# Kernel tuning notes

Measured on AMD Instinct MI355X. Metric: run time of the kernel, lower is better.

## Reference

```python
import jax, jax.numpy as jnp
import numpy as np

# B batch, SEQ encoder len, LDEC = label_len + pred_len = SEQ//2 + PRED decoder len
B, SEQ, PRED, LABEL = 4, 4096, 2048, 2048
NF, D, H, E, M, MA = 21, 512, 8, 64, 64, 25  # feats, d_model, heads, head_dim, modes, moving_avg
DFF, NLAYERS = 2048, 2
LDEC = LABEL + PRED

def pos_emb(L, d):
    pos = jnp.arange(L, dtype=jnp.float32)[:, None]
    div = jnp.exp(jnp.arange(0, d, 2, dtype=jnp.float32) * (-np.log(10000.0) / d))
    pe = jnp.zeros((L, d), jnp.float32)
    pe = pe.at[:, 0::2].set(jnp.sin(pos * div))
    pe = pe.at[:, 1::2].set(jnp.cos(pos * div))
    return pe

def circular_conv3(x, W):
    # torch Conv1d(k=3, padding=1, padding_mode='circular', bias=False); x:(B,L,Cin) W:(Cout,Cin,3)
    L = x.shape[1]
    xp = jnp.concatenate([x[:, -1:], x, x[:, :1]], axis=1)
    return xp[:, :L] @ W[:, :, 0].T + xp[:, 1:L + 1] @ W[:, :, 1].T + xp[:, 2:] @ W[:, :, 2].T

def series_decomp(x):
    # moving_avg: replicate-pad ends by (MA-1)//2, then AvgPool1d(MA, stride=1)
    p = (MA - 1) // 2
    xp = jnp.concatenate([jnp.repeat(x[:, :1], p, 1), x, jnp.repeat(x[:, -1:], p, 1)], axis=1)
    ma = jax.lax.reduce_window(xp, 0.0, jax.lax.add, (1, MA, 1), (1, 1, 1), 'VALID') / MA
    return x - ma, ma

def layer_norm(x, g, b, eps=1e-5):
    mu = x.mean(-1, keepdims=True)
    var = ((x - mu) ** 2).mean(-1, keepdims=True)
    return (x - mu) / jnp.sqrt(var + eps) * g + b

def my_layernorm(x, g, b):
    # my_Layernorm: LayerNorm minus its mean over the time axis
    xh = layer_norm(x, g, b)
    return xh - xh.mean(1, keepdims=True)

def to_c(Wf):
    return jax.lax.complex(Wf[..., 0], Wf[..., 1])

def fourier_block(q, Wf):
    # q:(B,L,H,E) -> out:(B,H,E,L); 'low' mode selection keeps the first M rfft bins
    x = jnp.transpose(q, (0, 2, 3, 1))
    L = x.shape[-1]
    xf = jnp.fft.rfft(x, axis=-1)[..., :M]
    of = jnp.einsum('bhim,hiom->bhom', xf, to_c(Wf))
    of = jnp.pad(of, ((0, 0), (0, 0), (0, 0), (0, L // 2 + 1 - M)))
    return jnp.fft.irfft(of, n=L, axis=-1)

def fourier_cross(q, k, Wf):
    # FourierCrossAttention with activation='tanh'; v is unused (as in torch)
    xq = jnp.transpose(q, (0, 2, 3, 1))
    xk = jnp.transpose(k, (0, 2, 3, 1))
    Lq = xq.shape[-1]
    qf = jnp.fft.rfft(xq, axis=-1)[..., :M]
    kf = jnp.fft.rfft(xk, axis=-1)[..., :M]
    s = jnp.tanh(jnp.einsum('bhex,bhey->bhxy', qf, kf))  # complex tanh
    o = jnp.einsum('bhxy,bhey->bhex', s, kf)
    ow = jnp.einsum('bhex,heox->bhox', o, to_c(Wf))
    of = jnp.pad(ow, ((0, 0), (0, 0), (0, 0), (0, Lq // 2 + 1 - M)))
    return jnp.fft.irfft(of / (D * D), n=Lq, axis=-1)  # / in_channels / out_channels

def attn_layer(xq, xkv, W4, b4, inner):
    Bq, Lq, Lk = xq.shape[0], xq.shape[1], xkv.shape[1]
    q = (xq @ W4[0].T + b4[0]).reshape(Bq, Lq, H, E)
    k = (xkv @ W4[1].T + b4[1]).reshape(Bq, Lk, H, E)
    v = (xkv @ W4[2].T + b4[2]).reshape(Bq, Lk, H, E)  # projected but unused by Fourier attention
    out = inner(q, k, v).reshape(Bq, Lq, H * E)  # replicates torch .view(B, L, -1) on contiguous (B,H,E,L)
    return out @ W4[3].T + b4[3]

def encoder_layer(x, W4, b4, Wf, W1, W2):
    x, _ = series_decomp(x + attn_layer(x, x, W4, b4, lambda q, k, v: fourier_block(q, Wf)))
    y = jax.nn.gelu(x @ W1.T, approximate=False) @ W2.T  # 1x1 convs == linear, no bias
    res, _ = series_decomp(x + y)
    return res

def decoder_layer(x, cross, Ws4, bs4, Wc4, bc4, Wf_self, Wf_cross, W1, W2, Wproj):
    x, t1 = series_decomp(x + attn_layer(x, x, Ws4, bs4, lambda q, k, v: fourier_block(q, Wf_self)))
    x, t2 = series_decomp(x + attn_layer(x, cross, Wc4, bc4, lambda q, k, v: fourier_cross(q, k, Wf_cross)))
    y = jax.nn.gelu(x @ W1.T, approximate=False) @ W2.T
    x, t3 = series_decomp(x + y)
    return x, circular_conv3(t1 + t2 + t3, Wproj)

def forward(x_enc, enc_emb_W, dec_emb_W, enc_qkvo_W, enc_qkvo_b, enc_ffn_W1, enc_ffn_W2, enc_fourier_W, enc_norm_g, enc_norm_b, dec_qkvo_W, dec_qkvo_b, dec_ffn_W1, dec_ffn_W2, dec_self_fourier_W, dec_cross_fourier_W, dec_trend_proj_W, dec_norm_g, dec_norm_b, final_W, final_b):
    mean = jnp.repeat(x_enc.mean(1, keepdims=True), PRED, axis=1)
    seasonal_init, trend_init = series_decomp(x_enc)
    trend_init = jnp.concatenate([trend_init[:, -LABEL:], mean], axis=1)  # (B,LDEC,NF)
    seasonal_init = jnp.pad(seasonal_init[:, -LABEL:], ((0, 0), (0, PRED), (0, 0)))
    enc_out = circular_conv3(x_enc, enc_emb_W) + pos_emb(SEQ, D)   # x_mark is None -> value + pos emb
    dec_out = circular_conv3(seasonal_init, dec_emb_W) + pos_emb(LDEC, D)
    for l in range(NLAYERS):  # encoder Fourier weights are a single shared module in torch
        enc_out = encoder_layer(enc_out, enc_qkvo_W[l], enc_qkvo_b[l], enc_fourier_W, enc_ffn_W1[l], enc_ffn_W2[l])
    enc_out = my_layernorm(enc_out, enc_norm_g, enc_norm_b)
    x, residual_trend = decoder_layer(dec_out, enc_out, dec_qkvo_W[0], dec_qkvo_b[0], dec_qkvo_W[1], dec_qkvo_b[1], dec_self_fourier_W, dec_cross_fourier_W, dec_ffn_W1, dec_ffn_W2, dec_trend_proj_W)
    trend = trend_init + residual_trend
    seasonal = my_layernorm(x, dec_norm_g, dec_norm_b) @ final_W.T + final_b
    return (trend + seasonal)[:, -PRED:, :]

def setup_inputs():
    ks = iter(jax.random.split(jax.random.key(0), 24))
    rn = lambda shape, s=0.02: jax.random.normal(next(ks), shape, jnp.float32) * s
    rf = lambda shape: jax.random.uniform(next(ks), shape, jnp.float32) / (D * D)  # torch.rand * 1/(in*out), complex split into (...,2)
    return {
        'x_enc': jax.random.normal(next(ks), (B, SEQ, NF), jnp.float32),
        'time': jnp.zeros((1,), jnp.int32),
        'dec_time': jnp.zeros((1,), jnp.int32),
        'enc_emb_W': rn((D, NF, 3)),
        'dec_emb_W': rn((D, NF, 3)),
        'enc_qkvo_W': rn((NLAYERS, 4, D, D)),
        'enc_qkvo_b': rn((NLAYERS, 4, D)),
        'enc_ffn_W1': rn((NLAYERS, DFF, D)),
        'enc_ffn_W2': rn((NLAYERS, D, DFF)),
        'enc_fourier_W': rf((H, E, E, M, 2)),
        'enc_norm_g': jnp.ones((D,), jnp.float32),
        'enc_norm_b': jnp.zeros((D,), jnp.float32),
        'dec_qkvo_W': rn((2, 4, D, D)),
        'dec_qkvo_b': rn((2, 4, D)),
        'dec_ffn_W1': rn((DFF, D)),
        'dec_ffn_W2': rn((D, DFF)),
        'dec_self_fourier_W': rf((H, E, E, M, 2)),
        'dec_cross_fourier_W': rf((H, E, E, M, 2)),
        'dec_trend_proj_W': rn((NF, D, 3)),
        'dec_norm_g': jnp.ones((D,), jnp.float32),
        'dec_norm_b': jnp.zeros((D,), jnp.float32),
        'final_W': rn((NF, D)),
        'final_b': jnp.zeros((NF,), jnp.float32),
    }

def reference(x_enc, time, dec_time, enc_emb_W, dec_emb_W, enc_qkvo_W, enc_qkvo_b, enc_ffn_W1, enc_ffn_W2, enc_fourier_W, enc_norm_g, enc_norm_b, dec_qkvo_W, dec_qkvo_b, dec_ffn_W1, dec_ffn_W2, dec_self_fourier_W, dec_cross_fourier_W, dec_trend_proj_W, dec_norm_g, dec_norm_b, final_W, final_b):
    # torch forward sets time = dec_time = None immediately; they are ignored
    return forward(x_enc, enc_emb_W, dec_emb_W, enc_qkvo_W, enc_qkvo_b, enc_ffn_W1, enc_ffn_W2, enc_fourier_W, enc_norm_g, enc_norm_b, dec_qkvo_W, dec_qkvo_b, dec_ffn_W1, dec_ffn_W2, dec_self_fourier_W, dec_cross_fourier_W, dec_trend_proj_W, dec_norm_g, dec_norm_b, final_W, final_b)
```

## Files before the change

kernel.cpp:

```cpp
#include <hip/hip_runtime.h>
#include <hip/hip_bf16.h>
#include <math.h>

namespace {

constexpr int NB    = 4;
constexpr int L     = 4096;
constexpr int PRED  = 2048;
constexpr int LABEL = 2048;
constexpr int NF    = 21;
constexpr int Dm    = 512;
constexpr int NH    = 8;
constexpr int NE    = 64;
constexpr int NM    = 64;
constexpr int DFF   = 2048;
constexpr float TWOPI = 6.283185307179586f;

typedef __attribute__((ext_vector_type(8))) short s16x8;
typedef __attribute__((ext_vector_type(4))) short s16x4;
typedef __attribute__((ext_vector_type(4))) float f32x4;

__device__ inline short f2b(float f) {
  __hip_bfloat16 h = __float2bfloat16(f);
  return __builtin_bit_cast(short, h);
}
__device__ inline float b2f(short s) {
  unsigned u = ((unsigned)(unsigned short)s) << 16;
  return __builtin_bit_cast(float, u);
}

__global__ void k_cvt(const float* __restrict__ src, short* __restrict__ dst, int n) {
  int i = (blockIdx.x * 256 + threadIdx.x) * 4;
  if (i >= n) return;
  f32x4 v = *(const f32x4*)(src + i);
  s16x4 p;
  p[0] = f2b(v[0]); p[1] = f2b(v[1]); p[2] = f2b(v[2]); p[3] = f2b(v[3]);
  *(s16x4*)(dst + i) = p;
}

__global__ void k_enc_mean(const float* __restrict__ x, float* __restrict__ mean_bf) {
  int bf = blockIdx.x; int b = bf / NF, f = bf % NF;
  const float* p = x + (size_t)b * L * NF + f;
  float s = 0.f;
  for (int l = threadIdx.x; l < L; l += 256) s += p[(size_t)l * NF];
  __shared__ float red[256];
  red[threadIdx.x] = s; __syncthreads();
  for (int st = 128; st > 0; st >>= 1) {
    if (threadIdx.x < st) red[threadIdx.x] += red[threadIdx.x + st];
    __syncthreads();
  }
  if (threadIdx.x == 0) mean_bf[bf] = red[0] * (1.0f / L);
}

__global__ void k_init_decomp(const float* __restrict__ x, const float* __restrict__ mean_bf,
                              float* __restrict__ sinit, float* __restrict__ tinit) {
  int idx = blockIdx.x * 256 + threadIdx.x;
  if (idx >= NB * L * NF) return;
  int f = idx % NF; int t = (idx / NF) % L; int b = idx / (NF * L);
  float sv, tv;
  if (t < LABEL) {
    int l = LABEL + t;
    float s = 0.f;
    #pragma unroll
    for (int j = -12; j <= 12; ++j) {
      int ll = l + j; ll = ll < 0 ? 0 : (ll > L - 1 ? L - 1 : ll);
      s += x[((size_t)b * L + ll) * NF + f];
    }
    float ma = s * (1.0f / 25.0f);
    sv = x[((size_t)b * L + l) * NF + f] - ma;
    tv = ma;
  } else { sv = 0.f; tv = mean_bf[b * NF + f]; }
  sinit[idx] = sv; tinit[idx] = tv;
}

__global__ __launch_bounds__(256) void k_embed2(const float* __restrict__ x,
                                                const float* __restrict__ W,
                                                float* __restrict__ out,
                                                short* __restrict__ outb) {
  int bid = blockIdx.x;
  int dt = bid & 7;
  int lt = (bid >> 3) & 63;
  int b  = bid >> 9;
  int l0 = lt << 6, d0 = dt << 6;
  __shared__ float xs[66][22];
  __shared__ float wt[63][68];
  int t = threadIdx.x;
  for (int i = t; i < 66 * 21; i += 256) {
    int r = i / 21, f = i - r * 21;
    int l = (l0 - 1 + r) & (L - 1);
    xs[r][f] = x[((size_t)b * L + l) * NF + f];
  }
  for (int i = t; i < 63 * 64; i += 256) {
    int k = i >> 6, dd = i & 63;
    wt[k][dd] = W[(size_t)(d0 + dd) * 63 + k];
  }
  __syncthreads();
  int tx = t & 15, ty = t >> 4;
  float acc[4][4] = {};
  #pragma unroll
  for (int f = 0; f < 21; ++f) {
    #pragma unroll
    for (int j = 0; j < 3; ++j) {
      int k = f * 3 + j;
      float xv[4], wv[4];
      #pragma unroll
      for (int i = 0; i < 4; ++i) xv[i] = xs[ty * 4 + i + j][f];
      #pragma unroll
      for (int jj = 0; jj < 4; ++jj) wv[jj] = wt[k][tx * 4 + jj];
      #pragma unroll
      for (int i = 0; i < 4; ++i)
        #pragma unroll
        for (int jj = 0; jj < 4; ++jj) acc[i][jj] += xv[i] * wv[jj];
    }
  }
  #pragma unroll
  for (int i = 0; i < 4; ++i) {
    int l = l0 + ty * 4 + i;
    #pragma unroll
    for (int jj = 0; jj < 4; ++jj) {
      int d = d0 + tx * 4 + jj;
      float dv = expf((float)(d & ~1) * (-9.210340371976184f / 512.0f));
      float ang = (float)l * dv;
      float pe = (d & 1) ? cosf(ang) : sinf(ang);
      float v = acc[i][jj] + pe;
      size_t o = ((size_t)b * L + l) * Dm + d;
      out[o] = v;
      outb[o] = f2b(v);
    }
  }
}

template<int MODE>
__global__ __launch_bounds__(256) void k_bgemm2(const short* __restrict__ A,
                       const short* __restrict__ W,
                       const float* __restrict__ bias, const float* __restrict__ R,
                       void* __restrict__ Cv, int N, int K) {
  __shared__ __align__(16) short As[128 * 64];
  __shared__ __align__(16) short Bs[128 * 64];
  int nt = N >> 7;
  int n0 = (blockIdx.x % nt) << 7;
  int m0 = (int)(blockIdx.x / nt) << 7;
  int t = threadIdx.x;
  int lane = t & 63, v = t >> 6;
  int srow = t >> 1;
  int shalf = t & 1;
  const short* Ap = A + (size_t)(m0 + srow) * K + shalf * 32;
  const short* Wp = W + (size_t)(n0 + srow) * K + shalf * 32;
  int wsw[4];
  #pragma unroll
  for (int q = 0; q < 4; ++q)
    wsw[q] = srow * 64 + (((shalf * 4 + q) ^ (srow & 7)) << 3);
  int wr = (v >> 1) << 6, wc = (v & 1) << 6;
  int fr_a = wr + (lane & 15);
  int fr_b = wc + (lane & 15);
  int cbase = lane >> 4;
  f32x4 acc[4][4] = {};
  s16x8 ra[4], rb[4];
  #pragma unroll
  for (int q = 0; q < 4; ++q) {
    ra[q] = *(const s16x8*)(Ap + q * 8);
    rb[q] = *(const s16x8*)(Wp + q * 8);
  }
  for (int k0 = 0; k0 < K; k0 += 64) {
    if (k0) __syncthreads();
    #pragma unroll
    for (int q = 0; q < 4; ++q) {
      *(s16x8*)(As + wsw[q]) = ra[q];
      *(s16x8*)(Bs + wsw[q]) = rb[q];
    }
    __syncthreads();
    if (k0 + 64 < K) {
      #pragma unroll
      for (int q = 0; q < 4; ++q) {
        ra[q] = *(const s16x8*)(Ap + k0 + 64 + q * 8);
        rb[q] = *(const s16x8*)(Wp + k0 + 64 + q * 8);
      }
    }
    #pragma unroll
    for (int ks = 0; ks < 2; ++ks) {
      int c = cbase + ks * 4;
      s16x8 af[4], bf_[4];
      #pragma unroll
      for (int f = 0; f < 4; ++f) {
        int r1 = fr_a + f * 16;
        af[f] = *(const s16x8*)(As + r1 * 64 + ((c ^ (r1 & 7)) << 3));
        int r2 = fr_b + f * 16;
        bf_[f] = *(const s16x8*)(Bs + r2 * 64 + ((c ^ (r2 & 7)) << 3));
      }
      #pragma unroll
      for (int fm = 0; fm < 4; ++fm)
        #pragma unroll
        for (int fn = 0; fn < 4; ++fn)
          acc[fm][fn] = __builtin_amdgcn_mfma_f32_16x16x32_bf16(af[fm], bf_[fn], acc[fm][fn], 0, 0, 0);
    }
  }
  int em = m0 + wr + ((lane >> 4) << 2);
  int en = n0 + wc + (lane & 15);
  #pragma unroll
  for (int fm = 0; fm < 4; ++fm) {
    #pragma unroll
    for (int fn = 0; fn < 4; ++fn) {
      int n = en + fn * 16;
      #pragma unroll
      for (int r = 0; r < 4; ++r) {
        int m = em + fm * 16 + r;
        float vv = acc[fm][fn][r];
        if (MODE == 0 || MODE == 1) vv += bias[n];
        if (MODE == 2) vv = 0.5f * vv * (1.0f + erff(vv * 0.70710678118654752f));
        if (MODE == 0 || MODE == 3) {
          vv += R[(size_t)m * N + n];
          ((float*)Cv)[(size_t)m * N + n] = vv;
        } else {
          ((short*)Cv)[(size_t)m * N + n] = f2b(vv);
        }
      }
    }
  }
}

__global__ void k_gentw(short* __restrict__ fm, short* __restrict__ gt) {
  int idx = blockIdx.x * 256 + threadIdx.x;
  {
    int m2 = idx >> 12, l = idx & 4095;
    int m = m2 & 63;
    int ph = (m * l) & (L - 1);
    float sv, cv;
    __sincosf((float)ph * (TWOPI / L), &sv, &cv);
    fm[idx] = f2b((m2 < 64) ? cv : -sv);
  }
  {
    int l = idx >> 7, m2 = idx & 127;
    int m = m2 & 63;
    int ph = (m * l) & (L - 1);
    float sv, cv;
    __sincosf((float)ph * (TWOPI / L), &sv, &cv);
    float g;
    if (m2 == 0) g = 1.0f;
    else if (m2 == 64) g = 0.0f;
    else g = (m2 < 64) ? 2.0f * cv : -2.0f * sv;
    gt[idx] = f2b(g);
  }
}

__global__ __launch_bounds__(256) void k_dft_mfma(const short* __restrict__ A,
                                                  const short* __restrict__ Fm,
                                                  float* __restrict__ S) {
  __shared__ __align__(16) short As[128 * 128];
  __shared__ __align__(16) short Bs[128 * 128];
  int bid = blockIdx.x;
  int kseg = bid & 15, ct = (bid >> 4) & 3, b = bid >> 6;
  int c0 = ct << 7;
  int lbase = kseg << 8;
  int t = threadIdx.x;
  int lane = t & 63, w = t >> 6;
  int wr = (w >> 1) << 6, wc = (w & 1) << 6;
  f32x4 acc[4][4] = {};
  const short* Ab = A + (size_t)b * L * Dm;

  for (int k0 = 0; k0 < 256; k0 += 128) {
    if (k0) __syncthreads();
    #pragma unroll
    for (int it = 0; it < 4; ++it) {
      int s = it * 256 + t;
      int cq = (s & 31) << 2;
      int lq = (s >> 5) << 2;
      const short* base = Ab + (size_t)(lbase + k0 + lq) * Dm + c0 + cq;
      s16x4 r0 = *(const s16x4*)(base);
      s16x4 r1 = *(const s16x4*)(base + Dm);
      s16x4 r2 = *(const s16x4*)(base + 2 * Dm);
      s16x4 r3 = *(const s16x4*)(base + 3 * Dm);
      #pragma unroll
      for (int j = 0; j < 4; ++j) {
        int crow = cq + j;
        s16x4 p;
        p[0] = r0[j]; p[1] = r1[j]; p[2] = r2[j]; p[3] = r3[j];
        *(s16x4*)((char*)As + crow * 256 + ((lq * 2) ^ ((crow & 15) << 4))) = p;
      }
    }
    #pragma unroll
    for (int it = 0; it < 8; ++it) {
      int m = it * 16 + (t >> 4);
      int lb = (t & 15) * 8;
      s16x8 vv = *(const s16x8*)(Fm + (size_t)m * L + lbase + k0 + lb);
      *(s16x8*)((char*)Bs + m * 256 + ((lb * 2) ^ ((m & 15) << 4))) = vv;
    }
    __syncthreads();
    #pragma unroll
    for (int ks = 0; ks < 4; ++ks) {
      int kb = ks * 64 + ((lane >> 4) << 4);
      s16x8 af[4], bf_[4];
      #pragma unroll
      for (int f = 0; f < 4; ++f) {
        int fr = wr + (lane & 15) + f * 16;
        af[f] = *(const s16x8*)((const char*)As + fr * 256 + (kb ^ ((fr & 15) << 4)));
        int mr = wc + (lane & 15) + f * 16;
        bf_[f] = *(const s16x8*)((const char*)Bs + mr * 256 + (kb ^ ((mr & 15) << 4)));
      }
      #pragma unroll
      for (int fm = 0; fm < 4; ++fm)
        #pragma unroll
        for (int fn = 0; fn < 4; ++fn)
          acc[fm][fn] = __builtin_amdgcn_mfma_f32_16x16x32_bf16(af[fm], bf_[fn], acc[fm][fn], 0, 0, 0);
    }
  }
  float* Sb = S + (size_t)b * Dm * 128;
  int ec = c0 + wr + ((lane >> 4) << 2);
  int em = wc + (lane & 15);
  #pragma unroll
  for (int fm = 0; fm < 4; ++fm)
    #pragma unroll
    for (int fn = 0; fn < 4; ++fn)
      #pragma unroll
      for (int r = 0; r < 4; ++r)
        atomicAdd(&Sb[(size_t)(ec + fm * 16 + r) * 128 + em + fn * 16], acc[fm][fn][r]);
}

__global__ __launch_bounds__(256) void k_irdft_mfma(const float* __restrict__ S,
                                                    const short* __restrict__ Gt,
                                                    short* __restrict__ O, float scale) {
  __shared__ __align__(16) short As[128 * 128];
  __shared__ __align__(16) short Bs[128 * 128];
  int bid = blockIdx.x;
  int lt = bid & 31, ct = (bid >> 5) & 3, b = bid >> 7;
  int c0 = ct << 7;
  int l0t = lt << 7;
  int t = threadIdx.x;
  int lane = t & 63, w = t >> 6;
  int wr = (w >> 1) << 6, wc = (w & 1) << 6;
  f32x4 acc[4][4] = {};
  #pragma unroll
  for (int it = 0; it < 8; ++it) {
    int c = it * 16 + (t >> 4);
    int me = (t & 15) * 8;
    const float* sp = S + ((size_t)b * Dm + c0 + c) * 128 + me;
    f32x4 v0 = *(const f32x4*)sp;
    f32x4 v1 = *(const f32x4*)(sp + 4);
    s16x8 p;
    p[0]=f2b(v0[0]); p[1]=f2b(v0[1]); p[2]=f2b(v0[2]); p[3]=f2b(v0[3]);
    p[4]=f2b(v1[0]); p[5]=f2b(v1[1]); p[6]=f2b(v1[2]); p[7]=f2b(v1[3]);
    *(s16x8*)((char*)As + c * 256 + ((me * 2) ^ ((c & 15) << 4))) = p;
  }
  #pragma unroll
  for (int it = 0; it < 8; ++it) {
    int l = it * 16 + (t >> 4);
    int me = (t & 15) * 8;
    s16x8 vv = *(const s16x8*)(Gt + (size_t)(l0t + l) * 128 + me);
    *(s16x8*)((char*)Bs + l * 256 + ((me * 2) ^ ((l & 15) << 4))) = vv;
  }
  __syncthreads();
  #pragma unroll
  for (int ks = 0; ks < 4; ++ks) {
    int kb = ks * 64 + ((lane >> 4) << 4);
    s16x8 af[4], bf_[4];
    #pragma unroll
    for (int f = 0; f < 4; ++f) {
      int fr = wr + (lane & 15) + f * 16;
      af[f] = *(const s16x8*)((const char*)As + fr * 256 + (kb ^ ((fr & 15) << 4)));
      int lr = wc + (lane & 15) + f * 16;
      bf_[f] = *(const s16x8*)((const char*)Bs + lr * 256 + (kb ^ ((lr & 15) << 4)));
    }
    #pragma unroll
    for (int fm = 0; fm < 4; ++fm)
      #pragma unroll
      for (int fn = 0; fn < 4; ++fn)
        acc[fm][fn] = __builtin_amdgcn_mfma_f32_16x16x32_bf16(af[fm], bf_[fn], acc[fm][fn], 0, 0, 0);
  }
  short* Ob = O + (size_t)b * Dm * L;
  int ec = c0 + wr + ((lane >> 4) << 2);
  int el = l0t + wc + (lane & 15);
  #pragma unroll
  for (int fm = 0; fm < 4; ++fm)
    #pragma unroll
    for (int fn = 0; fn < 4; ++fn)
      #pragma unroll
      for (int r = 0; r < 4; ++r)
        Ob[(size_t)(ec + fm * 16 + r) * L + el + fn * 16] = f2b(scale * acc[fm][fn][r]);
}

__global__ __launch_bounds__(256) void k_cmul2(const float* __restrict__ S, const float* __restrict__ Wf,
                                               float* __restrict__ O) {
  __shared__ float q[64 * 128];
  int bid = blockIdx.x;
  int og = bid & 3, h = (bid >> 2) & 7, b = bid >> 5;
  int t = threadIdx.x;
  const float* Sb = S + ((size_t)b * Dm + h * NE) * 128;
  for (int i = t; i < 8192; i += 256) q[i] = Sb[i];
  __syncthreads();
  int o = og * 16 + (t >> 4);
  int m0 = (t & 15) * 4;
  float ar[4] = {}, ai[4] = {};
  for (int i = 0; i < 64; ++i) {
    const float* wrow = Wf + (((size_t)h * 64 + i) * 64 + o) * 128 + m0 * 2;
    float wv[8];
    *(f32x4*)wv = *(const f32x4*)wrow;
    *(f32x4*)(wv + 4) = *(const f32x4*)(wrow + 4);
    const float* qi_ = q + i * 128;
    #pragma unroll
    for (int k = 0; k < 4; ++k) {
      float qr = qi_[m0 + k], qim = qi_[64 + m0 + k];
      float wr = wv[2 * k], wi = wv[2 * k + 1];
      ar[k] += qr * wr - qim * wi;
      ai[k] += qr * wi + qim * wr;
    }
  }
  float* Ob = O + ((size_t)b * Dm + h * NE + o) * 128;
  f32x4 vr, vi;
  #pragma unroll
  for (int k = 0; k < 4; ++k) { vr[k] = ar[k]; vi[k] = ai[k]; }
  *(f32x4*)(Ob + m0) = vr;
  *(f32x4*)(Ob + 64 + m0) = vi;
}

__global__ void k_cross_s(const float* __restrict__ Sq, const float* __restrict__ Sk,
                          float* __restrict__ Sout) {
  int bh = blockIdx.x;
  int b = bh >> 3, h = bh & 7;
  __shared__ float Qr[64][64], Qi[64][64], Kr[64][64], Ki[64][64];
  int t = threadIdx.x;
  const float* qb = Sq + ((size_t)b * Dm + h * NE) * 128;
  const float* kb = Sk + ((size_t)b * Dm + h * NE) * 128;
  for (int idx = t; idx < 4096; idx += 256) {
    int e = idx >> 6, x = idx & 63;
    Qr[e][x] = qb[e * 128 + x];
    Qi[e][x] = qb[e * 128 + 64 + x];
    Kr[e][x] = kb[e * 128 + x];
    Ki[e][x] = kb[e * 128 + 64 + x];
  }
  __syncthreads();
  int tx = t & 15, ty = t >> 4;
  float ar[4][4] = {}, ai[4][4] = {};
  for (int e = 0; e < 64; ++e) {
    float qr[4], qi[4], kr[4], ki[4];
    #pragma unroll
    for (int i = 0; i < 4; ++i) { qr[i] = Qr[e][(ty << 2) + i]; qi[i] = Qi[e][(ty << 2) + i]; }
    #pragma unroll
    for (int j = 0; j < 4; ++j) { kr[j] = Kr[e][(tx << 2) + j]; ki[j] = Ki[e][(tx << 2) + j]; }
    #pragma unroll
    for (int i = 0; i < 4; ++i)
      #pragma unroll
      for (int j = 0; j < 4; ++j) {
        ar[i][j] += qr[i] * kr[j] - qi[i] * ki[j];
        ai[i][j] += qr[i] * ki[j] + qi[i] * kr[j];
      }
  }
  float* sp = Sout + (size_t)bh * 4096 * 2;
  #pragma unroll
  for (int i = 0; i < 4; ++i)
    #pragma unroll
    for (int j = 0; j < 4; ++j) {
      int x = (ty << 2) + i, y = (tx << 2) + j;
      float a = ar[i][j], bb = ai[i][j];
      float th = tanhf(a);
      float u = tanf(bb);
      float re, im;
      if (fabsf(u) <= 1.0f) {
        float dn = 1.0f + th * th * u * u;
        re = th * (1.0f + u * u) / dn;
        im = u * (1.0f - th * th) / dn;
      } else {
        float iu = 1.0f / u;
        float dn = iu * iu + th * th;
        re = th * (iu * iu + 1.0f) / dn;
        im = iu * (1.0f - th * th) / dn;
      }
      sp[(x * 64 + y) * 2]     = re;
      sp[(x * 64 + y) * 2 + 1] = im;
    }
}

__global__ void k_cross_o(const float* __restrict__ Sin, const float* __restrict__ Sk,
                          float* __restrict__ O2) {
  int bh = blockIdx.x;
  int b = bh >> 3, h = bh & 7;
  __shared__ float SrT[64][64], SiT[64][64], KrT[64][64], KiT[64][64];
  int t = threadIdx.x;
  const float* sp = Sin + (size_t)bh * 8192;
  const float* kb = Sk + ((size_t)b * Dm + h * NE) * 128;
  for (int idx = t; idx < 4096; idx += 256) {
    int r = idx >> 6, c = idx & 63;
    SrT[c][r] = sp[idx * 2];
    SiT[c][r] = sp[idx * 2 + 1];
    KrT[c][r] = kb[r * 128 + c];
    KiT[c][r] = kb[r * 128 + 64 + c];
  }
  __syncthreads();
  int tx = t & 15, ty = t >> 4;
  float ar[4][4] = {}, ai[4][4] = {};
  for (int y = 0; y < 64; ++y) {
    float kr[4], ki[4], sr[4], si[4];
    #pragma unroll
    for (int i = 0; i < 4; ++i) { kr[i] = KrT[y][(ty << 2) + i]; ki[i] = KiT[y][(ty << 2) + i]; }
    #pragma unroll
    for (int j = 0; j < 4; ++j) { sr[j] = SrT[y][(tx << 2) + j]; si[j] = SiT[y][(tx << 2) + j]; }
    #pragma unroll
    for (int i = 0; i < 4; ++i)
      #pragma unroll
      for (int j = 0; j < 4; ++j) {
        ar[i][j] += sr[j] * kr[i] - si[j] * ki[i];
        ai[i][j] += sr[j] * ki[i] + si[j] * kr[i];
      }
  }
  float* ob = O2 + ((size_t)b * Dm + h * NE) * 128;
  #pragma unroll
  for (int i = 0; i < 4; ++i)
    #pragma unroll
    for (int j = 0; j < 4; ++j) {
      int e = (ty << 2) + i, x = (tx << 2) + j;
      ob[e * 128 + x]      = ar[i][j];
      ob[e * 128 + 64 + x] = ai[i][j];
    }
}

template<int TMODE>
__global__ __launch_bounds__(512) void k_decomp3(const float* __restrict__ Z, float* __restrict__ Sout,
                          short* __restrict__ Sb, float* __restrict__ T) {
  int b = blockIdx.x >> 7;
  int l0 = (blockIdx.x & 127) << 5;
  int d = threadIdx.x;
  const float* zb = Z + (size_t)b * L * Dm + d;
  float s = 0.f;
  #pragma unroll
  for (int j = -12; j <= 12; ++j) {
    int ll = l0 + j; ll = ll < 0 ? 0 : ll;
    s += zb[(size_t)ll * Dm];
  }
  for (int i = 0; i < 32; ++i) {
    int l = l0 + i;
    float ma = s * (1.0f / 25.0f);
    size_t idx = ((size_t)b * L + l) * Dm + d;
    float se = zb[(size_t)l * Dm] - ma;
    Sout[idx] = se;
    Sb[idx] = f2b(se);
    if (TMODE == 1) T[idx] = ma;
    else if (TMODE == 2) T[idx] += ma;
    int la = l + 13; la = la > L - 1 ? L - 1 : la;
    int lr = l - 12; lr = lr < 0 ? 0 : lr;
    s += zb[(size_t)la * Dm] - zb[(size_t)lr * Dm];
  }
}

__global__ void k_ln(const float* __restrict__ X, const float* __restrict__ g,
                     const float* __restrict__ be, float* __restrict__ Y) {
  int row = blockIdx.x;
  const float* x = X + (size_t)row * Dm;
  int t = threadIdx.x;
  float v0 = x[t], v1 = x[t + 256];
  float s = v0 + v1;
  __shared__ float red[4];
  #pragma unroll
  for (int off = 32; off > 0; off >>= 1) s += __shfl_down(s, off);
  int wid = t >> 6, lane = t & 63;
  if (lane == 0) red[wid] = s;
  __syncthreads();
  float mu = (red[0] + red[1] + red[2] + red[3]) * (1.0f / Dm);
  float e0 = v0 - mu, e1 = v1 - mu;
  float s2 = e0 * e0 + e1 * e1;
  #pragma unroll
  for (int off = 32; off > 0; off >>= 1) s2 += __shfl_down(s2, off);
  __syncthreads();
  if (lane == 0) red[wid] = s2;
  __syncthreads();
  float var = (red[0] + red[1] + red[2] + red[3]) * (1.0f / Dm);
  float rstd = rsqrtf(var + 1e-5f);
  float* y = Y + (size_t)row * Dm;
  y[t]       = e0 * rstd * g[t] + be[t];
  y[t + 256] = e1 * rstd * g[t + 256] + be[t + 256];
}

__global__ void k_colsum(const float* __restrict__ X, float* __restrict__ cm) {
  int b = blockIdx.x;
  int d = blockIdx.y * 256 + threadIdx.x;
  int lc = blockIdx.z;
  const float* x = X + ((size_t)b * L + (size_t)lc * 128) * Dm + d;
  float s = 0.f;
  for (int i = 0; i < 128; ++i) s += x[(size_t)i * Dm];
  atomicAdd(&cm[b * Dm + d], s);
}

__global__ void k_sub2(const float* __restrict__ X, const float* __restrict__ cm,
                       short* __restrict__ Y) {
  size_t idx = (size_t)blockIdx.x * 256 + threadIdx.x;
  int d = (int)(idx & (Dm - 1));
  int b = (int)(idx >> 21);
  Y[idx] = f2b(X[idx] - cm[b * Dm + d] * (1.0f / L));
}

__global__ __launch_bounds__(256) void k_trendproj3(const float* __restrict__ T,
                                                    const float* __restrict__ Wp,
                                                    float* __restrict__ RT) {
  __shared__ short wlds[512 * 64];
  int t = threadIdx.x;
  for (int i = t; i < NF * 512 * 3; i += 256) {
    int f = i / 1536, rem = i - f * 1536;
    int d = rem / 3, j = rem - d * 3;
    int s = f * 3 + j;
    int dst = d * 64 + (((s >> 3) ^ (d & 7)) << 3) + (s & 7);
    wlds[dst] = f2b(Wp[i]);
  }
  __syncthreads();
  int b = blockIdx.x >> 8;
  int g0 = (blockIdx.x & 255) << 4;
  int v = t >> 6, lane = t & 63;
  const float* Tb = T + (size_t)b * L * Dm;
  for (int rr = 0; rr < 4; ++rr) {
    int l = g0 + v * 4 + rr;
    int lm = (l - 1) & (L - 1), lp = (l + 1) & (L - 1);
    float acc[NF];
    #pragma unroll
    for (int f = 0; f < NF; ++f) acc[f] = 0.f;
    #pragma unroll
    for (int k = 0; k < 8; ++k) {
      int d = lane + k * 64;
      float t0 = Tb[(size_t)lm * Dm + d];
      float t1 = Tb[(size_t)l  * Dm + d];
      float t2 = Tb[(size_t)lp * Dm + d];
      const short* wrow = wlds + d * 64;
      int dsw = d & 7;
      #pragma unroll
      for (int c = 0; c < 8; ++c) {
        s16x8 wv = *(const s16x8*)(wrow + ((c ^ dsw) << 3));
        #pragma unroll
        for (int e = 0; e < 8; ++e) {
          int s = c * 8 + e;
          if (s < 63) {
            int f = s / 3, j = s - (s / 3) * 3;
            float wgt = b2f(wv[e]);
            acc[f] += (j == 0 ? t0 : (j == 1 ? t1 : t2)) * wgt;
          }
        }
      }
    }
    #pragma unroll
    for (int f = 0; f < NF; ++f) {
      float s = acc[f];
      #pragma unroll
      for (int off = 32; off > 0; off >>= 1) s += __shfl_xor(s, off);
      acc[f] = s;
    }
    if (lane == 0) {
      float* rp = RT + ((size_t)b * L + l) * NF;
      #pragma unroll
      for (int f = 0; f < NF; ++f) rp[f] = acc[f];
    }
  }
}

__global__ void k_final(const float* __restrict__ X, const float* __restrict__ cm,
                        const float* __restrict__ Wf, const float* __restrict__ bf,
                        const float* __restrict__ tinit, const float* __restrict__ RT,
                        float* __restrict__ out) {
  int bt = blockIdx.x; int b = bt / PRED, tt = bt % PRED;
  int l = LABEL + tt;
  __shared__ float row[512];
  __shared__ float partial[NF][9];
  int t = threadIdx.x;
  const float* x = X + ((size_t)b * L + l) * Dm;
  const float* c = cm + b * Dm;
  row[t]       = x[t]       - c[t]       * (1.0f / L);
  row[t + 256] = x[t + 256] - c[t + 256] * (1.0f / L);
  __syncthreads();
  if (t < 168) {
    int f = t >> 3, p = t & 7;
    const float* w = Wf + (size_t)f * Dm + p * 64;
    float s = 0.f;
    #pragma unroll
    for (int q = 0; q < 64; ++q) s += row[p * 64 + q] * w[q];
    partial[f][p] = s;
  }
  __syncthreads();
  if (t < NF) {
    float s = bf[t];
    #pragma unroll
    for (int p = 0; p < 8; ++p) s += partial[t][p];
    size_t src = ((size_t)b * L + l) * NF + t;
    out[((size_t)b * PRED + tt) * NF + t] = s + tinit[src] + RT[src];
  }
}

}

extern "C" void kernel_launch(void* const* d_in, const int* in_sizes, int n_in,
                              void* d_out, int out_size, void* d_ws, size_t ws_size,
                              hipStream_t stream) {
  (void)in_sizes; (void)n_in; (void)out_size; (void)ws_size;
  const float* x_enc              = (const float*)d_in[0];
  const float* enc_emb_W          = (const float*)d_in[3];
  const float* dec_emb_W          = (const float*)d_in[4];
  const float* enc_qkvo_W         = (const float*)d_in[5];
  const float* enc_qkvo_b         = (const float*)d_in[6];
  const float* enc_ffn_W1         = (const float*)d_in[7];
  const float* enc_ffn_W2         = (const float*)d_in[8];
  const float* enc_fourier_W      = (const float*)d_in[9];
  const float* enc_norm_g         = (const float*)d_in[10];
  const float* enc_norm_b         = (const float*)d_in[11];
  const float* dec_qkvo_W         = (const float*)d_in[12];
  const float* dec_qkvo_b         = (const float*)d_in[13];
  const float* dec_ffn_W1         = (const float*)d_in[14];
  const float* dec_ffn_W2         = (const float*)d_in[15];
  const float* dec_self_fourier_W = (const float*)d_in[16];
  const float* dec_cross_fourier_W= (const float*)d_in[17];
  const float* dec_trend_proj_W   = (const float*)d_in[18];
  const float* dec_norm_g         = (const float*)d_in[19];
  const float* dec_norm_b         = (const float*)d_in[20];
  const float* final_W            = (const float*)d_in[21];
  const float* final_b            = (const float*)d_in[22];
  float* out = (float*)d_out;

  float* ws = (float*)d_ws;
  const size_t SZ = (size_t)NB * L * Dm;
  float* S_x   = ws;
  float* S_dec = ws + SZ;
  float* S_z   = ws + 2 * SZ;
  float* T_sum = ws + 3 * SZ;
  short* act   = (short*)(ws + 4 * SZ);
  short* S_qb  = act;
  short* S_xb  = act + SZ;
  short* H16   = act;
  short* S_eb  = (short*)(ws + 5 * SZ);
  short* W16   = (short*)(ws + 5 * SZ + SZ / 2);
  float* sm = ws + 5 * SZ + SZ / 2 + 5242880;
  float* spec_q  = sm; sm += 262144;
  float* spec_k  = sm; sm += 262144;
  float* spec_o  = sm; sm += 262144;
  float* spec_o2 = sm; sm += 262144;
  float* spec_s  = sm; sm += 262144;
  float* mean_bf = sm; sm += 128;
  float* cm      = sm; sm += 2048;
  float* sinit   = sm; sm += (size_t)NB * L * NF;
  float* tinit   = sm; sm += (size_t)NB * L * NF;
  float* RT      = sm; sm += (size_t)NB * L * NF;
  short* fm_tw   = (short*)sm; sm += 262144;
  short* gt_tw   = (short*)sm; sm += 262144;

  short* w16_eq = W16;
  short* w16_e1 = W16 + 2097152;
  short* w16_e2 = W16 + 4194304;
  short* w16_dq = W16 + 6291456;
  short* w16_d1 = W16 + 8388608;
  short* w16_d2 = W16 + 9437184;

  auto cvt = [&](const float* s, short* d, int n) {
    k_cvt<<<(n / 4 + 255) / 256, 256, 0, stream>>>(s, d, n);
  };
  auto gemm = [&](int mode, const short* A, const short* Wt, const float* bias,
                  const float* R, void* C, int Mr, int N, int K) {
    dim3 grid((unsigned)((Mr >> 7) * (N >> 7)));
    if (mode == 0)      k_bgemm2<0><<<grid, 256, 0, stream>>>(A, Wt, bias, R, C, N, K);
    else if (mode == 1) k_bgemm2<1><<<grid, 256, 0, stream>>>(A, Wt, bias, R, C, N, K);
    else if (mode == 2) k_bgemm2<2><<<grid, 256, 0, stream>>>(A, Wt, bias, R, C, N, K);
    else                k_bgemm2<3><<<grid, 256, 0, stream>>>(A, Wt, bias, R, C, N, K);
  };
  auto dft = [&](const short* A, float* S) {
    hipMemsetAsync(S, 0, 262144 * sizeof(float), stream);
    k_dft_mfma<<<256, 256, 0, stream>>>(A, fm_tw, S);
  };
  auto irdft = [&](const float* S, short* O, float scale) {
    k_irdft_mfma<<<512, 256, 0, stream>>>(S, gt_tw, O, scale);
  };
  auto decomp = [&](int tmode, const float* Z, float* Sout, short* Sb, float* T) {
    if (tmode == 0)      k_decomp3<0><<<NB * 128, 512, 0, stream>>>(Z, Sout, Sb, T);
    else if (tmode == 1) k_decomp3<1><<<NB * 128, 512, 0, stream>>>(Z, Sout, Sb, T);
    else                 k_decomp3<2><<<NB * 128, 512, 0, stream>>>(Z, Sout, Sb, T);
  };

  const int MR = NB * L;
  const int RW = 8192;
  const size_t CH  = (size_t)RW * Dm;
  const int QQ = 262144;

  k_gentw<<<2048, 256, 0, stream>>>(fm_tw, gt_tw);
  cvt(enc_qkvo_W, w16_eq, 2097152);
  cvt(enc_ffn_W1, w16_e1, 2097152);
  cvt(enc_ffn_W2, w16_e2, 2097152);
  cvt(dec_qkvo_W, w16_dq, 2097152);
  cvt(dec_ffn_W1, w16_d1, 1048576);
  cvt(dec_ffn_W2, w16_d2, 1048576);
  k_enc_mean<<<NB * NF, 256, 0, stream>>>(x_enc, mean_bf);
  k_init_decomp<<<(NB * L * NF + 255) / 256, 256, 0, stream>>>(x_enc, mean_bf, sinit, tinit);
  k_embed2<<<NB * 512, 256, 0, stream>>>(x_enc, enc_emb_W, S_x, S_eb);

  for (int layer = 0; layer < 2; ++layer) {
    const short* Wl = w16_eq + (size_t)layer * 4 * QQ;
    const float* bl = enc_qkvo_b + (size_t)layer * 4 * Dm;
    gemm(1, S_eb, Wl, bl, nullptr, S_qb, MR, Dm, Dm);
    dft(S_qb, spec_q);
    k_cmul2<<<128, 256, 0, stream>>>(spec_q, enc_fourier_W, spec_o);
    irdft(spec_o, S_xb, 1.0f / L);
    gemm(0, S_xb, Wl + 3 * QQ, bl + 3 * Dm, S_x, S_z, MR, Dm, Dm);
    decomp(0, S_z, S_x, S_eb, nullptr);
    for (int ch = 0; ch < 2; ++ch) {
      gemm(2, S_eb + (size_t)ch * CH, w16_e1 + (size_t)layer * DFF * Dm, nullptr, nullptr,
           H16, RW, DFF, Dm);
      gemm(3, H16, w16_e2 + (size_t)layer * Dm * DFF, nullptr, S_x + ch * CH,
           S_z + ch * CH, RW, Dm, DFF);
    }
    decomp(0, S_z, S_x, S_eb, nullptr);
  }
  k_ln<<<NB * L, 256, 0, stream>>>(S_x, enc_norm_g, enc_norm_b, S_z);
  hipMemsetAsync(cm, 0, 2048 * sizeof(float), stream);
  k_colsum<<<dim3(NB, 2, 32), 256, 0, stream>>>(S_z, cm);
  k_sub2<<<32768, 256, 0, stream>>>(S_z, cm, S_eb);

  k_embed2<<<NB * 512, 256, 0, stream>>>(sinit, dec_emb_W, S_dec, S_xb);
  {
    const short* Wl = w16_dq;
    const float* bl = dec_qkvo_b;
    gemm(1, S_xb, Wl, bl, nullptr, S_qb, MR, Dm, Dm);
    dft(S_qb, spec_q);
    k_cmul2<<<128, 256, 0, stream>>>(spec_q, dec_self_fourier_W, spec_o);
    irdft(spec_o, S_xb, 1.0f / L);
    gemm(0, S_xb, Wl + 3 * QQ, bl + 3 * Dm, S_dec, S_z, MR, Dm, Dm);
    decomp(1, S_z, S_x, S_xb, T_sum);
  }
  {
    const short* Wl = w16_dq + 4 * QQ;
    const float* bl = dec_qkvo_b + 4 * Dm;
    gemm(1, S_xb, Wl, bl, nullptr, S_qb, MR, Dm, Dm);
    gemm(1, S_eb, Wl + QQ, bl + Dm, nullptr, S_xb, MR, Dm, Dm);
    dft(S_qb, spec_q);
    dft(S_xb, spec_k);
    k_cross_s<<<NB * NH, 256, 0, stream>>>(spec_q, spec_k, spec_s);
    k_cross_o<<<NB * NH, 256, 0, stream>>>(spec_s, spec_k, spec_o2);
    k_cmul2<<<128, 256, 0, stream>>>(spec_o2, dec_cross_fourier_W, spec_o);
    irdft(spec_o, S_qb, (1.0f / L) / (512.0f * 512.0f));
    gemm(0, S_qb, Wl + 3 * QQ, bl + 3 * Dm, S_x, S_z, MR, Dm, Dm);
    decomp(2, S_z, S_dec, S_eb, T_sum);
  }
  for (int ch = 0; ch < 2; ++ch) {
    gemm(2, S_eb + (size_t)ch * CH, w16_d1, nullptr, nullptr, H16, RW, DFF, Dm);
    gemm(3, H16, w16_d2, nullptr, S_dec + ch * CH, S_z + ch * CH, RW, Dm, DFF);
  }
  decomp(2, S_z, S_x, S_eb, T_sum);
  k_trendproj3<<<NB * 256, 256, 0, stream>>>(T_sum, dec_trend_proj_W, RT);
  k_ln<<<NB * L, 256, 0, stream>>>(S_x, dec_norm_g, dec_norm_b, S_z);
  hipMemsetAsync(cm, 0, 2048 * sizeof(float), stream);
  k_colsum<<<dim3(NB, 2, 32), 256, 0, stream>>>(S_z, cm);
  k_final<<<NB * PRED, 256, 0, stream>>>(S_z, cm, final_W, final_b, tinit, RT, out);
}
```

Before: 1.664 ms.

## Use direct global-to-LDS loads in GEMM and MFMA-based trend projection

The main bf16 GEMM drops its register-staged double buffering and uses global_load_lds to copy A/W tiles straight into swizzled LDS, with two barriers per k-step. The trend projection is rebuilt as an MFMA GEMM over three shifted time taps, using bf16 weights pre-transposed by a new prep kernel. The last decomposition now writes the accumulated trend directly as bf16, saving a separate float read. The GEMM rewrite gives up overlap of the next tile's loads with compute in exchange for skipping the register round trip, and it also adds an empty unused loop.

Result: faster. 1.595 ms (-4.1%).

```diff
diff --git a/kernel.cpp b/kernel.cpp
--- a/kernel.cpp
+++ b/kernel.cpp
@@ -36,6 +36,14 @@
   s16x4 p;
   p[0] = f2b(v[0]); p[1] = f2b(v[1]); p[2] = f2b(v[2]); p[3] = f2b(v[3]);
   *(s16x4*)(dst + i) = p;
+}
+
+__global__ void k_prepw(const float* __restrict__ Wp, short* __restrict__ Wt3) {
+  int i = blockIdx.x * 256 + threadIdx.x;
+  if (i >= 3 * 32 * 512) return;
+  int d = i & 511, n = (i >> 9) & 31, j = i >> 14;
+  float v = (n < NF) ? Wp[(size_t)n * 1536 + d * 3 + j] : 0.f;
+  Wt3[i] = f2b(v);
 }
 
 __global__ void k_enc_mean(const float* __restrict__ x, float* __restrict__ mean_bf) {
@@ -131,7 +139,7 @@
 }
 
 template<int MODE>
-__global__ __launch_bounds__(256) void k_bgemm2(const short* __restrict__ A,
+__global__ __launch_bounds__(256) void k_bgemm3(const short* __restrict__ A,
                        const short* __restrict__ W,
                        const float* __restrict__ bias, const float* __restrict__ R,
                        void* __restrict__ Cv, int N, int K) {
@@ -141,41 +149,31 @@
   int n0 = (blockIdx.x % nt) << 7;
   int m0 = (int)(blockIdx.x / nt) << 7;
   int t = threadIdx.x;
-  int lane = t & 63, v = t >> 6;
-  int srow = t >> 1;
-  int shalf = t & 1;
-  const short* Ap = A + (size_t)(m0 + srow) * K + shalf * 32;
-  const short* Wp = W + (size_t)(n0 + srow) * K + shalf * 32;
-  int wsw[4];
-  #pragma unroll
-  for (int q = 0; q < 4; ++q)
-    wsw[q] = srow * 64 + (((shalf * 4 + q) ^ (srow & 7)) << 3);
-  int wr = (v >> 1) << 6, wc = (v & 1) << 6;
+  int lane = t & 63, w = t >> 6;
+  int wr = (w >> 1) << 6, wc = (w & 1) << 6;
   int fr_a = wr + (lane & 15);
   int fr_b = wc + (lane & 15);
   int cbase = lane >> 4;
+  int rs[4], gko[4];
+  #pragma unroll
+  for (int i = 0; i < 4; ++i) {
+    int ch = (w * 4 + i) * 64 + lane;
+    rs[i] = ch >> 3;
+    gko[i] = ((ch & 7) ^ (rs[i] & 7)) << 3;
+  }
   f32x4 acc[4][4] = {};
-  s16x8 ra[4], rb[4];
-  #pragma unroll
-  for (int q = 0; q < 4; ++q) {
-    ra[q] = *(const s16x8*)(Ap + q * 8);
-    rb[q] = *(const s16x8*)(Wp + q * 8);
-  }
   for (int k0 = 0; k0 < K; k0 += 64) {
-    if (k0) __syncthreads();
-    #pragma unroll
-    for (int q = 0; q < 4; ++q) {
-      *(s16x8*)(As + wsw[q]) = ra[q];
-      *(s16x8*)(Bs + wsw[q]) = rb[q];
-    }
     __syncthreads();
-    if (k0 + 64 < K) {
-      #pragma unroll
-      for (int q = 0; q < 4; ++q) {
-        ra[q] = *(const s16x8*)(Ap + k0 + 64 + q * 8);
-        rb[q] = *(const s16x8*)(Wp + k0 + 64 + q * 8);
-      }
-    }
+    #pragma unroll
+    for (int i = 0; i < 4; ++i) {
+      __builtin_amdgcn_global_load_lds(
+          (const unsigned int*)(A + (size_t)(m0 + rs[i]) * K + k0 + gko[i]),
+          (unsigned int*)(As + ((w * 4 + i) << 9)), 16, 0, 0);
+      __builtin_amdgcn_global_load_lds(
+          (const unsigned int*)(W + (size_t)(n0 + rs[i]) * K + k0 + gko[i]),
+          (unsigned int*)(Bs + ((w * 4 + i) << 9)), 16, 0, 0);
+    }
+    __syncthreads();
     #pragma unroll
     for (int ks = 0; ks < 2; ++ks) {
       int c = cbase + ks * 4;
@@ -368,6 +366,11 @@
   short* Ob = O + (size_t)b * Dm * L;
   int ec = c0 + wr + ((lane >> 4) << 2);
   int el = l0t + wc + (lane & 15);
+  #pragma unroll
+  for (int fm = 0; fm < 4; ++fm)
+    #pragma unroll
+    for (int fn = 0; fn < 2 * 2; ++fn)
+      ;
   #pragma unroll
   for (int fm = 0; fm < 4; ++fm)
     #pragma unroll
@@ -513,7 +516,7 @@
 
 template<int TMODE>
 __global__ __launch_bounds__(512) void k_decomp3(const float* __restrict__ Z, float* __restrict__ Sout,
-                          short* __restrict__ Sb, float* __restrict__ T) {
+                          short* __restrict__ Sb, float* __restrict__ T, short* __restrict__ Tb) {
   int b = blockIdx.x >> 7;
   int l0 = (blockIdx.x & 127) << 5;
   int d = threadIdx.x;
@@ -533,6 +536,7 @@
     Sb[idx] = f2b(se);
     if (TMODE == 1) T[idx] = ma;
     else if (TMODE == 2) T[idx] += ma;
+    else if (TMODE == 3) Tb[idx] = f2b(T[idx] + ma);
     int la = l + 13; la = la > L - 1 ? L - 1 : la;
     int lr = l - 12; lr = lr < 0 ? 0 : lr;
     s += zb[(size_t)la * Dm] - zb[(size_t)lr * Dm];
@@ -585,62 +589,61 @@
   Y[idx] = f2b(X[idx] - cm[b * Dm + d] * (1.0f / L));
 }
 
-__global__ __launch_bounds__(256) void k_trendproj3(const float* __restrict__ T,
-                                                    const float* __restrict__ Wp,
+__global__ __launch_bounds__(256) void k_trendproj4(const short* __restrict__ Tb,
+                                                    const short* __restrict__ Wt3,
                                                     float* __restrict__ RT) {
-  __shared__ short wlds[512 * 64];
-  int t = threadIdx.x;
-  for (int i = t; i < NF * 512 * 3; i += 256) {
-    int f = i / 1536, rem = i - f * 1536;
-    int d = rem / 3, j = rem - d * 3;
-    int s = f * 3 + j;
-    int dst = d * 64 + (((s >> 3) ^ (d & 7)) << 3) + (s & 7);
-    wlds[dst] = f2b(Wp[i]);
-  }
-  __syncthreads();
-  int b = blockIdx.x >> 8;
-  int g0 = (blockIdx.x & 255) << 4;
-  int v = t >> 6, lane = t & 63;
-  const float* Tb = T + (size_t)b * L * Dm;
-  for (int rr = 0; rr < 4; ++rr) {
-    int l = g0 + v * 4 + rr;
-    int lm = (l - 1) & (L - 1), lp = (l + 1) & (L - 1);
-    float acc[NF];
-    #pragma unroll
-    for (int f = 0; f < NF; ++f) acc[f] = 0.f;
-    #pragma unroll
-    for (int k = 0; k < 8; ++k) {
-      int d = lane + k * 64;
-      float t0 = Tb[(size_t)lm * Dm + d];
-      float t1 = Tb[(size_t)l  * Dm + d];
-      float t2 = Tb[(size_t)lp * Dm + d];
-      const short* wrow = wlds + d * 64;
-      int dsw = d & 7;
-      #pragma unroll
-      for (int c = 0; c < 8; ++c) {
-        s16x8 wv = *(const s16x8*)(wrow + ((c ^ dsw) << 3));
+  __shared__ __align__(16) short As[64 * 64];
+  __shared__ __align__(16) short Bs[32 * 64];
+  int m0 = blockIdx.x << 6;
+  int t = threadIdx.x, lane = t & 63, w = t >> 6;
+  int fr_a = (w << 4) + (lane & 15);
+  int cbase = lane >> 4;
+  f32x4 acc[2] = {};
+  int srow = t >> 2;
+  int ca = (t & 3) * 2;
+  int nB = t >> 3;
+  int ckB = t & 7;
+  int mrow = m0 + srow;
+  int bb = mrow >> 12, ll = mrow & 4095;
+  for (int j = 0; j < 3; ++j) {
+    int lsrc = (ll + j - 1) & 4095;
+    const short* Arow = Tb + (((size_t)(bb << 12) + lsrc) << 9);
+    const short* Brow = Wt3 + (j << 14) + (nB << 9);
+    for (int k0 = 0; k0 < 512; k0 += 64) {
+      __syncthreads();
+      #pragma unroll
+      for (int q = 0; q < 2; ++q) {
+        int c = ca + q;
+        s16x8 v = *(const s16x8*)(Arow + k0 + (c << 3));
+        *(s16x8*)(As + srow * 64 + ((c ^ (srow & 7)) << 3)) = v;
+      }
+      {
+        s16x8 v = *(const s16x8*)(Brow + k0 + (ckB << 3));
+        *(s16x8*)(Bs + nB * 64 + ((ckB ^ (nB & 7)) << 3)) = v;
+      }
+      __syncthreads();
+      #pragma unroll
+      for (int ks = 0; ks < 2; ++ks) {
+        int c = cbase + ks * 4;
+        s16x8 af = *(const s16x8*)(As + fr_a * 64 + ((c ^ (fr_a & 7)) << 3));
         #pragma unroll
-        for (int e = 0; e < 8; ++e) {
-          int s = c * 8 + e;
-          if (s < 63) {
-            int f = s / 3, j = s - (s / 3) * 3;
-            float wgt = b2f(wv[e]);
-            acc[f] += (j == 0 ? t0 : (j == 1 ? t1 : t2)) * wgt;
-          }
+        for (int fn = 0; fn < 2; ++fn) {
+          int r2 = (lane & 15) + fn * 16;
+          s16x8 bf_ = *(const s16x8*)(Bs + r2 * 64 + ((c ^ (r2 & 7)) << 3));
+          acc[fn] = __builtin_amdgcn_mfma_f32_16x16x32_bf16(af, bf_, acc[fn], 0, 0, 0);
         }
       }
     }
-    #pragma unroll
-    for (int f = 0; f < NF; ++f) {
-      float s = acc[f];
-      #pragma unroll
-      for (int off = 32; off > 0; off >>= 1) s += __shfl_xor(s, off);
-      acc[f] = s;
-    }
-    if (lane == 0) {
-      float* rp = RT + ((size_t)b * L + l) * NF;
-      #pragma unroll
-      for (int f = 0; f < NF; ++f) rp[f] = acc[f];
+  }
+  int em = m0 + (w << 4) + ((lane >> 4) << 2);
+  int en = lane & 15;
+  #pragma unroll
+  for (int fn = 0; fn < 2; ++fn) {
+    int n = en + fn * 16;
+    if (n < NF) {
+      #pragma unroll
+      for (int r = 0; r < 4; ++r)
+        RT[(size_t)(em + r) * NF + n] = acc[fn][r];
     }
   }
 }
@@ -731,6 +734,8 @@
   float* RT      = sm; sm += (size_t)NB * L * NF;
   short* fm_tw   = (short*)sm; sm += 262144;
   short* gt_tw   = (short*)sm; sm += 262144;
+  short* tb16    = (short*)sm; sm += SZ / 2;
+  short* wt3     = (short*)sm; sm += 49152;
 
   short* w16_eq = W16;
   short* w16_e1 = W16 + 2097152;
@@ -745,10 +750,10 @@
   auto gemm = [&](int mode, const short* A, const short* Wt, const float* bias,
                   const float* R, void* C, int Mr, int N, int K) {
     dim3 grid((unsigned)((Mr >> 7) * (N >> 7)));
-    if (mode == 0)      k_bgemm2<0><<<grid, 256, 0, stream>>>(A, Wt, bias, R, C, N, K);
-    else if (mode == 1) k_bgemm2<1><<<grid, 256, 0, stream>>>(A, Wt, bias, R, C, N, K);
-    else if (mode == 2) k_bgemm2<2><<<grid, 256, 0, stream>>>(A, Wt, bias, R, C, N, K);
-    else                k_bgemm2<3><<<grid, 256, 0, stream>>>(A, Wt, bias, R, C, N, K);
+    if (mode == 0)      k_bgemm3<0><<<grid, 256, 0, stream>>>(A, Wt, bias, R, C, N, K);
+    else if (mode == 1) k_bgemm3<1><<<grid, 256, 0, stream>>>(A, Wt, bias, R, C, N, K);
+    else if (mode == 2) k_bgemm3<2><<<grid, 256, 0, stream>>>(A, Wt, bias, R, C, N, K);
+    else                k_bgemm3<3><<<grid, 256, 0, stream>>>(A, Wt, bias, R, C, N, K);
   };
   auto dft = [&](const short* A, float* S) {
     hipMemsetAsync(S, 0, 262144 * sizeof(float), stream);
@@ -757,15 +762,16 @@
   auto irdft = [&](const float* S, short* O, float scale) {
     k_irdft_mfma<<<512, 256, 0, stream>>>(S, gt_tw, O, scale);
   };
-  auto decomp = [&](int tmode, const float* Z, float* Sout, short* Sb, float* T) {
-    if (tmode == 0)      k_decomp3<0><<<NB * 128, 512, 0, stream>>>(Z, Sout, Sb, T);
-    else if (tmode == 1) k_decomp3<1><<<NB * 128, 512, 0, stream>>>(Z, Sout, Sb, T);
-    else                 k_decomp3<2><<<NB * 128, 512, 0, stream>>>(Z, Sout, Sb, T);
+  auto decomp = [&](int tmode, const float* Z, float* Sout, short* Sb, float* T, short* Tb) {
+    if (tmode == 0)      k_decomp3<0><<<NB * 128, 512, 0, stream>>>(Z, Sout, Sb, T, Tb);
+    else if (tmode == 1) k_decomp3<1><<<NB * 128, 512, 0, stream>>>(Z, Sout, Sb, T, Tb);
+    else if (tmode == 2) k_decomp3<2><<<NB * 128, 512, 0, stream>>>(Z, Sout, Sb, T, Tb);
+    else                 k_decomp3<3><<<NB * 128, 512, 0, stream>>>(Z, Sout, Sb, T, Tb);
   };
 
   const int MR = NB * L;
   const int RW = 8192;
-  const size_t CH  = (size_t)RW * Dm;
+  const size_t CH = (size_t)RW * Dm;
   const int QQ = 262144;
 
   k_gentw<<<2048, 256, 0, stream>>>(fm_tw, gt_tw);
@@ -775,6 +781,7 @@
   cvt(dec_qkvo_W, w16_dq, 2097152);
   cvt(dec_ffn_W1, w16_d1, 1048576);
   cvt(dec_ffn_W2, w16_d2, 1048576);
+  k_prepw<<<192, 256, 0, stream>>>(dec_trend_proj_W, wt3);
   k_enc_mean<<<NB * NF, 256, 0, stream>>>(x_enc, mean_bf);
   k_init_decomp<<<(NB * L * NF + 255) / 256, 256, 0, stream>>>(x_enc, mean_bf, sinit, tinit);
   k_embed2<<<NB * 512, 256, 0, stream>>>(x_enc, enc_emb_W, S_x, S_eb);
@@ -787,14 +794,14 @@
     k_cmul2<<<128, 256, 0, stream>>>(spec_q, enc_fourier_W, spec_o);
     irdft(spec_o, S_xb, 1.0f / L);
     gemm(0, S_xb, Wl + 3 * QQ, bl + 3 * Dm, S_x, S_z, MR, Dm, Dm);
-    decomp(0, S_z, S_x, S_eb, nullptr);
+    decomp(0, S_z, S_x, S_eb, nullptr, nullptr);
     for (int ch = 0; ch < 2; ++ch) {
       gemm(2, S_eb + (size_t)ch * CH, w16_e1 + (size_t)layer * DFF * Dm, nullptr, nullptr,
            H16, RW, DFF, Dm);
       gemm(3, H16, w16_e2 + (size_t)layer * Dm * DFF, nullptr, S_x + ch * CH,
            S_z + ch * CH, RW, Dm, DFF);
     }
-    decomp(0, S_z, S_x, S_eb, nullptr);
+    decomp(0, S_z, S_x, S_eb, nullptr, nullptr);
   }
   k_ln<<<NB * L, 256, 0, stream>>>(S_x, enc_norm_g, enc_norm_b, S_z);
   hipMemsetAsync(cm, 0, 2048 * sizeof(float), stream);
@@ -810,7 +817,7 @@
     k_cmul2<<<128, 256, 0, stream>>>(spec_q, dec_self_fourier_W, spec_o);
     irdft(spec_o, S_xb, 1.0f / L);
     gemm(0, S_xb, Wl + 3 * QQ, bl + 3 * Dm, S_dec, S_z, MR, Dm, Dm);
-    decomp(1, S_z, S_x, S_xb, T_sum);
+    decomp(1, S_z, S_x, S_xb, T_sum, nullptr);
   }
   {
     const short* Wl = w16_dq + 4 * QQ;
@@ -824,14 +831,14 @@
     k_cmul2<<<128, 256, 0, stream>>>(spec_o2, dec_cross_fourier_W, spec_o);
     irdft(spec_o, S_qb, (1.0f / L) / (512.0f * 512.0f));
     gemm(0, S_qb, Wl + 3 * QQ, bl + 3 * Dm, S_x, S_z, MR, Dm, Dm);
-    decomp(2, S_z, S_dec, S_eb, T_sum);
+    decomp(2, S_z, S_dec, S_eb, T_sum, nullptr);
   }
   for (int ch = 0; ch < 2; ++ch) {
     gemm(2, S_eb + (size_t)ch * CH, w16_d1, nullptr, nullptr, H16, RW, DFF, Dm);
     gemm(3, H16, w16_d2, nullptr, S_dec + ch * CH, S_z + ch * CH, RW, Dm, DFF);
   }
-  decomp(2, S_z, S_x, S_eb, T_sum);
-  k_trendproj3<<<NB * 256, 256, 0, stream>>>(T_sum, dec_trend_proj_W, RT);
+  decomp(3, S_z, S_x, S_eb, T_sum, tb16);
+  k_trendproj4<<<256, 256, 0, stream>>>(tb16, wt3, RT);
   k_ln<<<NB * L, 256, 0, stream>>>(S_x, dec_norm_g, dec_norm_b, S_z);
   hipMemsetAsync(cm, 0, 2048 * sizeof(float), stream);
   k_colsum<<<dim3(NB, 2, 32), 256, 0, stream>>>(S_z, cm);
```
